# Optimization experiments

Hardware: AMD Instinct MI355X
Metric: run time of the kernel (lower is better)

Reference implementation:

```python
import jax, jax.numpy as jnp
import numpy as np

N = 3072      # number of EDU nodes in the document
H = 256       # opt.tree_hid_him
NREL = 18     # relation classes (hardcoded in rel_clf)
ALPHA = 0.25


def setup_inputs() -> dict:
    key = jax.random.key(0)
    ks = jax.random.split(key, 20)
    s = 0.02
    all_edus = jax.random.normal(ks[0], (1, N, H), jnp.float32)
    # dependency tree: child i (1..N-1) has parent < i
    children_ids = jnp.arange(1, N, dtype=jnp.int32)
    parents_ids = (jax.random.randint(ks[1], (N - 1,), 0, N) % jnp.maximum(children_ids, 1)).astype(jnp.int32)
    half = (N - 1) // 2
    left_adj = jnp.zeros((N, N), jnp.float32).at[parents_ids[:half], children_ids[:half]].set(1.0)
    right_adj = jnp.zeros((N, N), jnp.float32).at[parents_ids[half:], children_ids[half:]].set(1.0)
    rels = jax.random.randint(ks[2], (N - 1,), 1, NREL).astype(jnp.int32)  # all nonzero -> rels[rels!=0] == rels
    return dict(
        all_edus=all_edus,
        left_adj=left_adj,
        right_adj=right_adj,
        W_bilin=jax.random.normal(ks[3], (2, H, H), jnp.float32) * s,
        b_bilin=jnp.zeros((2,), jnp.float32),
        W_head=jax.random.normal(ks[4], (2, H), jnp.float32) * s,
        W_dep=jax.random.normal(ks[5], (2, H), jnp.float32) * s,
        Wr1=jax.random.normal(ks[6], (H, H), jnp.float32) * s,
        br1=jnp.zeros((H,), jnp.float32),
        Wr2=jax.random.normal(ks[7], (H, 1), jnp.float32) * s,
        br2=jnp.zeros((1,), jnp.float32),
        Wrel1=jax.random.normal(ks[8], (2 * H, H), jnp.float32) * s,
        brel1=jnp.zeros((H,), jnp.float32),
        Wrel2=jax.random.normal(ks[9], (H, NREL), jnp.float32) * s,
        brel2=jnp.zeros((NREL,), jnp.float32),
        children_ids=children_ids,
        parents_ids=parents_ids,
        rels=rels,
        true_root=0,
    )


def reference(all_edus, left_adj, right_adj, W_bilin, b_bilin, W_head, W_dep,
              Wr1, br1, Wr2, br2, Wrel1, brel1, Wrel2, brel2,
              children_ids, parents_ids, rels, true_root):
    x = all_edus[0]                                      # [N, H]
    # --- get_compat_matrix: compat[i, j, k] = bilin_k(h_i, h_j) + head_k(h_i) + dep_k(h_j) ---
    compat = (jnp.einsum('ih,khd,jd->ijk', x, W_bilin, x) + b_bilin
              + (x @ W_head.T)[:, None, :] + (x @ W_dep.T)[None, :, :])  # [N, N, 2]
    # --- root_clf ---
    g = jax.nn.gelu(x @ Wr1 + br1, approximate=False)
    root_scores = g @ Wr2 + br2                          # [N, 1]
    # --- logistic_loss (matrix-tree theorem) ---
    gold = (root_scores[true_root, 0]
            + jnp.sum(compat[:, :, 0] * left_adj)
            + jnp.sum(compat[:, :, 1] * right_adj))
    A = jnp.exp(compat).sum(axis=-1)                     # [N, N]
    lap = jnp.diag(A.sum(axis=0)) - A                    # diag of column sums (torch sum over dim=1)
    lap = lap.at[0, :].set(jnp.exp(root_scores[:, 0]))
    sign, logabs = jnp.linalg.slogdet(lap)
    logdet = jnp.where(sign > 0, logabs, jnp.nan)        # torch.logdet semantics
    notnan = ((~jnp.isnan(gold)) & (~jnp.isnan(logdet))).astype(lap.dtype)
    mask = (gold <= logdet * notnan).astype(lap.dtype)
    loss = (logdet - gold) * mask
    loss = jnp.where(jnp.isnan(loss), 0.0, loss)
    log_loss = ALPHA * loss
    # --- rels_loss: edge-indexed gather + MLP + CE(sum) ---
    feats = jnp.concatenate([x[parents_ids], x[children_ids]], axis=1)  # [E, 2H]
    h = jax.nn.gelu(feats @ Wrel1 + brel1, approximate=False)
    logits = h @ Wrel2 + brel2                           # [E, 18]
    logp = jax.nn.log_softmax(logits, axis=-1)
    ce = -jnp.sum(jnp.take_along_axis(logp, rels[:, None].astype(jnp.int32), axis=1))
    return log_loss + ce
```

## Files before the change

### kernel.cpp

```cpp
#include <hip/hip_runtime.h>
#include <math.h>

#define N 3072
#define H 256
#define NRELS 18
#define EDGES (N-1)
#define HALF ((N-1)/2)
#define NB 64
#define NSTEP (N/NB)

static const size_t OFF_M   = 0;
static const size_t OFF_Y   = (size_t)N*N;
static const size_t OFF_XH  = OFF_Y + (size_t)4*N*H;
static const size_t OFF_XD  = OFF_XH + (size_t)2*N;
static const size_t OFF_RS  = OFF_XD + (size_t)2*N;
static const size_t OFF_CS  = OFF_RS + (size_t)N;
static const size_t OFF_ACC = OFF_CS + (size_t)N;
static const size_t OFF_IAC = OFF_ACC + 8;

__device__ __forceinline__ float gelu_exact(float a){
    return 0.5f*a*(1.0f + erff(a*0.70710678118654752440f));
}

__global__ void k_init(float* cs, float* acc, int* iacc){
    int t = blockIdx.x*256 + threadIdx.x;
    if(t < N) cs[t] = 0.f;
    if(t < 8) acc[t] = 0.f;
    if(t < 4) iacc[t] = 0;
}

__global__ __launch_bounds__(256) void k_xhd(const float* __restrict__ x,
        const float* __restrict__ Wh, const float* __restrict__ Wd,
        float* __restrict__ xh, float* __restrict__ xd){
    __shared__ float xs[H];
    int i = blockIdx.x, t = threadIdx.x;
    xs[t] = x[(size_t)i*H + t];
    __syncthreads();
    int w = t >> 6, lane = t & 63;
    const float* Wrow = (w==0)? Wh : (w==1)? Wh+H : (w==2)? Wd : Wd+H;
    float s = 0.f;
    #pragma unroll
    for(int q=0;q<4;q++) s += xs[lane+64*q]*Wrow[lane+64*q];
    #pragma unroll
    for(int off=32;off>0;off>>=1) s += __shfl_down(s, off, 64);
    if(lane==0){ if(w<2) xh[i*2+w]=s; else xd[i*2+(w-2)]=s; }
}

__global__ __launch_bounds__(256) void k_root(const float* __restrict__ x,
        const float* __restrict__ Wr1, const float* __restrict__ br1,
        const float* __restrict__ Wr2, const float* __restrict__ br2,
        float* __restrict__ rs){
    __shared__ float xs[H];
    __shared__ float red[256];
    int i = blockIdx.x, t = threadIdx.x;
    xs[t] = x[(size_t)i*H + t];
    __syncthreads();
    float a = br1[t];
    for(int d=0; d<H; d++) a += xs[d]*Wr1[(size_t)d*H + t];
    red[t] = gelu_exact(a)*Wr2[t];
    __syncthreads();
    for(int s=128;s>0;s>>=1){ if(t<s) red[t]+=red[t+s]; __syncthreads(); }
    if(t==0) rs[i] = red[0] + br2[0];
}

__global__ __launch_bounds__(256) void k_mats(const float* __restrict__ x,
        const float* __restrict__ Wb, const float* __restrict__ Wrel1,
        float* __restrict__ Yout){
    __shared__ float xs[H];
    int i = blockIdx.x, m = blockIdx.y, t = threadIdx.x;
    xs[t] = x[(size_t)i*H + t];
    __syncthreads();
    const float* W = (m==0)? Wb : (m==1)? Wb + (size_t)H*H
                   : (m==2)? Wrel1 : Wrel1 + (size_t)H*H;
    float acc = 0.f;
    for(int h=0; h<H; h++) acc += xs[h]*W[(size_t)h*H + t];
    Yout[(size_t)m*N*H + (size_t)i*H + t] = acc;
}

__global__ __launch_bounds__(256) void k_compatA(
        const float* __restrict__ x, const float* __restrict__ Y0,
        const float* __restrict__ Y1, const float* __restrict__ xh,
        const float* __restrict__ xd, const float* __restrict__ bb,
        float* __restrict__ M){
    __shared__ float a0s[16][65], a1s[16][65], bs[16][65];
    int i0 = blockIdx.y*64, j0 = blockIdx.x*64;
    int t = threadIdx.x;
    int tx = t & 15, ty = t >> 4;
    float c0[4][4] = {}, c1[4][4] = {};
    for(int k0=0; k0<H; k0+=16){
        int kk = t & 15, r0 = t >> 4;
        for(int rr=r0; rr<64; rr+=16){
            a0s[kk][rr] = Y0[(size_t)(i0+rr)*H + k0+kk];
            a1s[kk][rr] = Y1[(size_t)(i0+rr)*H + k0+kk];
            bs [kk][rr] = x [(size_t)(j0+rr)*H + k0+kk];
        }
        __syncthreads();
        #pragma unroll
        for(int kk2=0; kk2<16; kk2++){
            float ar0[4], ar1[4], br[4];
            #pragma unroll
            for(int u=0;u<4;u++){ ar0[u]=a0s[kk2][ty*4+u]; ar1[u]=a1s[kk2][ty*4+u]; }
            #pragma unroll
            for(int v=0;v<4;v++) br[v]=bs[kk2][tx*4+v];
            #pragma unroll
            for(int u=0;u<4;u++)
                #pragma unroll
                for(int v=0;v<4;v++){ c0[u][v]+=ar0[u]*br[v]; c1[u][v]+=ar1[u]*br[v]; }
        }
        __syncthreads();
    }
    float b0 = bb[0], b1 = bb[1];
    #pragma unroll
    for(int u=0;u<4;u++){
        int i = i0 + ty*4 + u;
        float h0 = xh[2*i], h1 = xh[2*i+1];
        int pi = (i==0)? N-1 : i-1;
        #pragma unroll
        for(int v=0;v<4;v++){
            int j = j0 + tx*4 + v;
            int pj = (j==0)? N-1 : j-1;
            float cc0 = c0[u][v] + b0 + h0 + xd[2*j];
            float cc1 = c1[u][v] + b1 + h1 + xd[2*j+1];
            M[(size_t)pi*N + pj] = -(expf(cc0)+expf(cc1));
        }
    }
}

__global__ __launch_bounds__(256) void k_gold(const float* __restrict__ x,
        const float* __restrict__ Y, const float* __restrict__ xh,
        const float* __restrict__ xd, const float* __restrict__ bb,
        const int* __restrict__ par, const int* __restrict__ chi,
        float* __restrict__ acc){
    int w = threadIdx.x >> 6, lane = threadIdx.x & 63;
    int e = blockIdx.x*4 + w;
    if(e >= EDGES) return;
    int p = par[e], c = chi[e];
    int k = (e < HALF)? 0 : 1;
    const float* Yk = Y + (size_t)k*N*H;
    float s = 0.f;
    #pragma unroll
    for(int q=0;q<4;q++)
        s += Yk[(size_t)p*H + lane+64*q]*x[(size_t)c*H + lane+64*q];
    #pragma unroll
    for(int off=32;off>0;off>>=1) s += __shfl_down(s, off, 64);
    if(lane==0) atomicAdd(acc+0, s + bb[k] + xh[2*p+k] + xd[2*c+k]);
}

__global__ __launch_bounds__(256) void k_ce(
        const float* __restrict__ Pm, const float* __restrict__ Qm,
        const float* __restrict__ brel1, const float* __restrict__ Wrel2,
        const float* __restrict__ brel2, const int* __restrict__ par,
        const int* __restrict__ chi, const int* __restrict__ rels,
        float* __restrict__ acc){
    __shared__ float red[256][NRELS+1];
    int e = blockIdx.x, t = threadIdx.x;
    int p = par[e], c = chi[e];
    float a = Pm[(size_t)p*H + t] + Qm[(size_t)c*H + t] + brel1[t];
    float h = gelu_exact(a);
    #pragma unroll
    for(int r=0;r<NRELS;r++) red[t][r] = h*Wrel2[t*NRELS + r];
    __syncthreads();
    for(int s=128;s>0;s>>=1){
        if(t<s){
            #pragma unroll
            for(int r=0;r<NRELS;r++) red[t][r] += red[t+s][r];
        }
        __syncthreads();
    }
    if(t==0){
        int rsel = rels[e];
        float mx = -1e30f;
        for(int r=0;r<NRELS;r++) mx = fmaxf(mx, red[0][r]+brel2[r]);
        float se = 0.f;
        for(int r=0;r<NRELS;r++) se += expf(red[0][r]+brel2[r]-mx);
        float lse = mx + logf(se);
        atomicAdd(acc+2, lse - (red[0][rsel]+brel2[rsel]));
    }
}

__global__ __launch_bounds__(256) void k_colsum(const float* __restrict__ M,
        float* __restrict__ cs){
    int c = blockIdx.x*256 + threadIdx.x;
    int r0 = blockIdx.y*(N/16);
    float s = 0.f;
    for(int r=r0; r<r0+N/16; r++) s += M[(size_t)r*N + c];
    atomicAdd(cs+c, s);
}

__global__ __launch_bounds__(256) void k_fix(float* __restrict__ M,
        const float* __restrict__ cs, const float* __restrict__ rs){
    int c = blockIdx.x*256 + threadIdx.x;
    if(c < N-1) M[(size_t)c*N + c] -= cs[c];
    int oj = (c==N-1)? 0 : c+1;
    M[(size_t)(N-1)*N + c] = expf(rs[oj]);
}

__global__ __launch_bounds__(256) void k_lu_diag(float* __restrict__ M, int K0,
        float* __restrict__ acc, int* __restrict__ iacc){
    __shared__ float D[NB][NB+1];
    __shared__ float lcol[NB];
    int t = threadIdx.x;
    for(int e=t; e<NB*NB; e+=256){ int r=e>>6, c=e&63; D[r][c] = M[(size_t)(K0+r)*N + K0+c]; }
    __syncthreads();
    for(int j=0;j<NB;j++){
        if(t>j && t<NB){ float l = D[t][j]/D[j][j]; D[t][j]=l; lcol[t]=l; }
        __syncthreads();
        int ty = t>>4, tx = t&15;
        for(int ii=j+1+ty; ii<NB; ii+=16){
            float l = lcol[ii];
            for(int cc=j+1+tx; cc<NB; cc+=16) D[ii][cc] -= l*D[j][cc];
        }
        __syncthreads();
    }
    if(t==0){
        float s = 0.f; int neg=0, zer=0;
        for(int j=0;j<NB;j++){
            float v = D[j][j];
            s += logf(fabsf(v));
            if(v < 0.f) neg++;
            if(v == 0.f) zer++;
        }
        atomicAdd(acc+1, s);
        if(neg) atomicAdd(iacc+0, neg);
        if(zer) atomicAdd(iacc+1, zer);
    }
    __syncthreads();
    for(int e=t; e<NB*NB; e+=256){ int r=e>>6, c=e&63; M[(size_t)(K0+r)*N + K0+c] = D[r][c]; }
}

__global__ __launch_bounds__(128) void k_lu_panel(float* __restrict__ M, int K0){
    __shared__ float Dd[NB][NB+1];
    __shared__ float Tl[128][NB+1];
    int t = threadIdx.x;
    int m = N - K0 - NB;
    int nch = (m + 127)/128;
    for(int e=t; e<NB*NB; e+=128){ int r=e>>6, c=e&63; Dd[r][c] = M[(size_t)(K0+r)*N + K0+c]; }
    __syncthreads();
    if((int)blockIdx.x < nch){
        int base = K0 + NB + blockIdx.x*128;
        for(int e=t; e<128*NB; e+=128){ int rr=e>>6, cc=e&63;
            int row = base+rr; Tl[rr][cc] = (row<N)? M[(size_t)row*N + K0+cc] : 0.f; }
        __syncthreads();
        int row = base + t;
        if(row < N){
            float a[NB];
            #pragma unroll
            for(int c=0;c<NB;c++) a[c] = Tl[t][c];
            #pragma unroll
            for(int c=0;c<NB;c++){
                float xc = a[c]/Dd[c][c];
                a[c] = xc;
                #pragma unroll
                for(int cc=c+1;cc<NB;cc++) a[cc] -= xc*Dd[c][cc];
            }
            #pragma unroll
            for(int c=0;c<NB;c++) Tl[t][c] = a[c];
        }
        __syncthreads();
        for(int e=t; e<128*NB; e+=128){ int rr=e>>6, cc=e&63;
            int row2 = base+rr; if(row2<N) M[(size_t)row2*N + K0+cc] = Tl[rr][cc]; }
    } else {
        int cbase = K0 + NB + (blockIdx.x - nch)*128;
        for(int e=t; e<NB*128; e+=128){ int rr=e>>7, cc=e&127;
            int col = cbase+cc; Tl[cc][rr] = (col<N)? M[(size_t)(K0+rr)*N + col] : 0.f; }
        __syncthreads();
        int col = cbase + t;
        if(col < N){
            float a[NB];
            #pragma unroll
            for(int r=0;r<NB;r++) a[r] = Tl[t][r];
            #pragma unroll
            for(int r=0;r<NB;r++){
                float ur = a[r];
                #pragma unroll
                for(int rr=r+1;rr<NB;rr++) a[rr] -= ur*Dd[rr][r];
            }
            #pragma unroll
            for(int r=0;r<NB;r++) Tl[t][r] = a[r];
        }
        __syncthreads();
        for(int e=t; e<NB*128; e+=128){ int rr=e>>7, cc=e&127;
            int col2 = cbase+cc; if(col2<N) M[(size_t)(K0+rr)*N + col2] = Tl[cc][rr]; }
    }
}

__global__ __launch_bounds__(256) void k_lu_update(float* __restrict__ M, int K0){
    __shared__ float As[16][65], Bs[16][65];
    int base = K0 + NB;
    int ii0 = base + blockIdx.y*64;
    int jj0 = base + blockIdx.x*64;
    int t = threadIdx.x, tx = t&15, ty = t>>4;
    float c[4][4] = {};
    for(int k0=0; k0<NB; k0+=16){
        {
            int kk = t&15, r0 = t>>4;
            for(int rr=r0; rr<64; rr+=16)
                As[kk][rr] = M[(size_t)(ii0+rr)*N + K0+k0+kk];
        }
        {
            int cc = t&63, kr = t>>6;
            for(int k2=kr; k2<16; k2+=4)
                Bs[k2][cc] = M[(size_t)(K0+k0+k2)*N + jj0+cc];
        }
        __syncthreads();
        #pragma unroll
        for(int kk2=0; kk2<16; kk2++){
            float ar[4], br[4];
            #pragma unroll
            for(int u=0;u<4;u++) ar[u] = As[kk2][ty*4+u];
            #pragma unroll
            for(int v=0;v<4;v++) br[v] = Bs[kk2][tx*4+v];
            #pragma unroll
            for(int u=0;u<4;u++)
                #pragma unroll
                for(int v=0;v<4;v++) c[u][v] += ar[u]*br[v];
        }
        __syncthreads();
    }
    #pragma unroll
    for(int u=0;u<4;u++)
        #pragma unroll
        for(int v=0;v<4;v++){
            size_t idx = (size_t)(ii0+ty*4+u)*N + jj0+tx*4+v;
            M[idx] -= c[u][v];
        }
}

__global__ void k_final(const float* __restrict__ acc, const int* __restrict__ iacc,
        const float* __restrict__ rs, const int* __restrict__ troot,
        float* __restrict__ out){
    float gold = acc[0] + rs[troot[0]];
    float logabs = acc[1];
    bool pos = (iacc[1]==0) && ((iacc[0]&1)==0);
    float logdet = pos ? logabs : __builtin_nanf("");
    float notnan = (!isnan(gold) && !isnan(logdet)) ? 1.f : 0.f;
    float mv = logdet*notnan;
    float mask = (gold <= mv) ? 1.f : 0.f;
    float loss = (logdet - gold)*mask;
    if(isnan(loss)) loss = 0.f;
    out[0] = 0.25f*loss + acc[2];
}

extern "C" void kernel_launch(void* const* d_in, const int* in_sizes, int n_in,
                              void* d_out, int out_size, void* d_ws, size_t ws_size,
                              hipStream_t stream){
    const float* x     = (const float*)d_in[0];
    const float* Wb    = (const float*)d_in[3];
    const float* bb    = (const float*)d_in[4];
    const float* Wh    = (const float*)d_in[5];
    const float* Wd    = (const float*)d_in[6];
    const float* Wr1   = (const float*)d_in[7];
    const float* br1   = (const float*)d_in[8];
    const float* Wr2   = (const float*)d_in[9];
    const float* br2   = (const float*)d_in[10];
    const float* Wrel1 = (const float*)d_in[11];
    const float* brel1 = (const float*)d_in[12];
    const float* Wrel2 = (const float*)d_in[13];
    const float* brel2 = (const float*)d_in[14];
    const int* chi   = (const int*)d_in[15];
    const int* par   = (const int*)d_in[16];
    const int* rels  = (const int*)d_in[17];
    const int* troot = (const int*)d_in[18];

    float* ws = (float*)d_ws;
    float* M  = ws + OFF_M;
    float* Y  = ws + OFF_Y;
    float* Y0 = Y;
    float* Y1 = Y + (size_t)N*H;
    float* Pm = Y + (size_t)2*N*H;
    float* Qm = Y + (size_t)3*N*H;
    float* xh = ws + OFF_XH;
    float* xd = ws + OFF_XD;
    float* rs = ws + OFF_RS;
    float* cs = ws + OFF_CS;
    float* acc = ws + OFF_ACC;
    int*   iacc = (int*)(ws + OFF_IAC);
    float* out = (float*)d_out;

    k_init<<<N/256, 256, 0, stream>>>(cs, acc, iacc);
    k_xhd<<<N, 256, 0, stream>>>(x, Wh, Wd, xh, xd);
    k_root<<<N, 256, 0, stream>>>(x, Wr1, br1, Wr2, br2, rs);
    k_mats<<<dim3(N,4), 256, 0, stream>>>(x, Wb, Wrel1, Y);
    k_compatA<<<dim3(N/64, N/64), 256, 0, stream>>>(x, Y0, Y1, xh, xd, bb, M);
    k_gold<<<(EDGES+3)/4, 256, 0, stream>>>(x, Y, xh, xd, bb, par, chi, acc);
    k_ce<<<EDGES, 256, 0, stream>>>(Pm, Qm, brel1, Wrel2, brel2, par, chi, rels, acc);
    k_colsum<<<dim3(N/256, 16), 256, 0, stream>>>(M, cs);
    k_fix<<<N/256, 256, 0, stream>>>(M, cs, rs);

    k_lu_diag<<<1, 256, 0, stream>>>(M, 0, acc, iacc);
    for(int kb=0; kb<NSTEP-1; kb++){
        int K0 = kb*NB;
        int m  = N - K0 - NB;
        int nch = (m + 127)/128;
        k_lu_panel<<<2*nch, 128, 0, stream>>>(M, K0);
        dim3 g(m/64, m/64);
        k_lu_update<<<g, 256, 0, stream>>>(M, K0);
        k_lu_diag<<<1, 256, 0, stream>>>(M, K0+NB, acc, iacc);
    }
    k_final<<<1, 1, 0, stream>>>(acc, iacc, rs, troot, out);
}
```

Baseline: 5.498 ms.

## Replace LU panel triangular solves with explicit block inverses and fuse diag factorization

The 64x64 diagonal block factorization now also builds explicit inverses of U and L and stores them in the no-longer-needed Y scratch area. The panel step becomes a small GEMM against those inverses instead of per-thread sequential triangular solves. The next diagonal block is factored inside block (0,0) of the trailing-update kernel, which removes one launch per step. Loads are vectorized with float4. In exchange, explicit inversion is slightly less numerically stable, and block (0,0) now lengthens the update kernel's critical path.

```diff
diff --git a/kernel.cpp b/kernel.cpp
--- a/kernel.cpp
+++ b/kernel.cpp
@@ -195,27 +195,26 @@
     M[(size_t)(N-1)*N + c] = expf(rs[oj]);
 }
 
-__global__ __launch_bounds__(256) void k_lu_diag(float* __restrict__ M, int K0,
-        float* __restrict__ acc, int* __restrict__ iacc){
-    __shared__ float D[NB][NB+1];
-    __shared__ float lcol[NB];
+__device__ __forceinline__ void factor_invert_64(
+        float (*Ds)[NB+1], float (*Xs)[NB+1], float (*Ys)[NB+1],
+        float* __restrict__ Uinv, float* __restrict__ Linv,
+        float* __restrict__ acc, int* __restrict__ iacc,
+        float* lcol ){
     int t = threadIdx.x;
-    for(int e=t; e<NB*NB; e+=256){ int r=e>>6, c=e&63; D[r][c] = M[(size_t)(K0+r)*N + K0+c]; }
-    __syncthreads();
     for(int j=0;j<NB;j++){
-        if(t>j && t<NB){ float l = D[t][j]/D[j][j]; D[t][j]=l; lcol[t]=l; }
+        if(t>j && t<NB){ float l = Ds[t][j]/Ds[j][j]; Ds[t][j]=l; lcol[t]=l; }
         __syncthreads();
         int ty = t>>4, tx = t&15;
         for(int ii=j+1+ty; ii<NB; ii+=16){
             float l = lcol[ii];
-            for(int cc=j+1+tx; cc<NB; cc+=16) D[ii][cc] -= l*D[j][cc];
+            for(int cc=j+1+tx; cc<NB; cc+=16) Ds[ii][cc] -= l*Ds[j][cc];
         }
         __syncthreads();
     }
     if(t==0){
         float s = 0.f; int neg=0, zer=0;
         for(int j=0;j<NB;j++){
-            float v = D[j][j];
+            float v = Ds[j][j];
             s += logf(fabsf(v));
             if(v < 0.f) neg++;
             if(v == 0.f) zer++;
@@ -225,105 +224,161 @@
         if(zer) atomicAdd(iacc+1, zer);
     }
     __syncthreads();
-    for(int e=t; e<NB*NB; e+=256){ int r=e>>6, c=e&63; M[(size_t)(K0+r)*N + K0+c] = D[r][c]; }
-}
-
-__global__ __launch_bounds__(128) void k_lu_panel(float* __restrict__ M, int K0){
-    __shared__ float Dd[NB][NB+1];
-    __shared__ float Tl[128][NB+1];
+    if(t < NB){
+        int c = t;
+        for(int r=NB-1;r>=0;r--){
+            float v;
+            if(r > c) v = 0.f;
+            else {
+                v = (r==c)? 1.f : 0.f;
+                for(int j=r+1;j<=c;j++) v -= Ds[r][j]*Xs[j][c];
+                v /= Ds[r][r];
+            }
+            Xs[r][c] = v;
+        }
+        for(int r=0;r<NB;r++) Uinv[r*NB+c] = Xs[r][c];
+    } else if(t < 2*NB){
+        int c = t - NB;
+        for(int r=0;r<NB;r++){
+            float v;
+            if(r < c) v = 0.f;
+            else if(r == c) v = 1.f;
+            else {
+                v = 0.f;
+                for(int j=c;j<r;j++) v -= Ds[r][j]*Ys[j][c];
+            }
+            Ys[r][c] = v;
+        }
+        for(int r=0;r<NB;r++) Linv[r*NB+c] = Ys[r][c];
+    }
+}
+
+__global__ __launch_bounds__(256) void k_lu_diag0(const float* __restrict__ M,
+        float* __restrict__ Uinv, float* __restrict__ Linv,
+        float* __restrict__ acc, int* __restrict__ iacc){
+    __shared__ float Ds[NB][NB+1], Xs[NB][NB+1], Ys[NB][NB+1];
+    __shared__ float lcol[NB];
     int t = threadIdx.x;
-    int m = N - K0 - NB;
-    int nch = (m + 127)/128;
-    for(int e=t; e<NB*NB; e+=128){ int r=e>>6, c=e&63; Dd[r][c] = M[(size_t)(K0+r)*N + K0+c]; }
-    __syncthreads();
-    if((int)blockIdx.x < nch){
-        int base = K0 + NB + blockIdx.x*128;
-        for(int e=t; e<128*NB; e+=128){ int rr=e>>6, cc=e&63;
-            int row = base+rr; Tl[rr][cc] = (row<N)? M[(size_t)row*N + K0+cc] : 0.f; }
-        __syncthreads();
-        int row = base + t;
-        if(row < N){
-            float a[NB];
-            #pragma unroll
-            for(int c=0;c<NB;c++) a[c] = Tl[t][c];
-            #pragma unroll
-            for(int c=0;c<NB;c++){
-                float xc = a[c]/Dd[c][c];
-                a[c] = xc;
-                #pragma unroll
-                for(int cc=c+1;cc<NB;cc++) a[cc] -= xc*Dd[c][cc];
-            }
-            #pragma unroll
-            for(int c=0;c<NB;c++) Tl[t][c] = a[c];
-        }
-        __syncthreads();
-        for(int e=t; e<128*NB; e+=128){ int rr=e>>6, cc=e&63;
-            int row2 = base+rr; if(row2<N) M[(size_t)row2*N + K0+cc] = Tl[rr][cc]; }
+    for(int e=t; e<NB*NB; e+=256){ int r=e>>6, c=e&63; Ds[r][c] = M[(size_t)r*N + c]; }
+    __syncthreads();
+    factor_invert_64(Ds, Xs, Ys, Uinv, Linv, acc, iacc, lcol);
+}
+
+__global__ __launch_bounds__(256) void k_lu_panel(float* __restrict__ M, int K0,
+        const float* __restrict__ Uinv, const float* __restrict__ Linv){
+    __shared__ float As[NB][NB+1], Bs[NB][NB+1];
+    int t = threadIdx.x;
+    int base = K0 + NB;
+    int nt = (N - base)/NB;
+    bool isL = ((int)blockIdx.x < nt);
+    int bi = isL ? blockIdx.x : blockIdx.x - nt;
+
+    int lr = t >> 4, lc4 = (t & 15)*4;
+    if(isL){
+        int ii0 = base + bi*NB;
+        #pragma unroll
+        for(int q=0;q<4;q++){
+            int r = lr + 16*q;
+            float4 v = *(const float4*)&M[(size_t)(ii0+r)*N + K0 + lc4];
+            As[r][lc4]=v.x; As[r][lc4+1]=v.y; As[r][lc4+2]=v.z; As[r][lc4+3]=v.w;
+            float4 u = *(const float4*)&Uinv[r*NB + lc4];
+            Bs[r][lc4]=u.x; Bs[r][lc4+1]=u.y; Bs[r][lc4+2]=u.z; Bs[r][lc4+3]=u.w;
+        }
     } else {
-        int cbase = K0 + NB + (blockIdx.x - nch)*128;
-        for(int e=t; e<NB*128; e+=128){ int rr=e>>7, cc=e&127;
-            int col = cbase+cc; Tl[cc][rr] = (col<N)? M[(size_t)(K0+rr)*N + col] : 0.f; }
-        __syncthreads();
-        int col = cbase + t;
-        if(col < N){
-            float a[NB];
-            #pragma unroll
-            for(int r=0;r<NB;r++) a[r] = Tl[t][r];
-            #pragma unroll
-            for(int r=0;r<NB;r++){
-                float ur = a[r];
-                #pragma unroll
-                for(int rr=r+1;rr<NB;rr++) a[rr] -= ur*Dd[rr][r];
-            }
-            #pragma unroll
-            for(int r=0;r<NB;r++) Tl[t][r] = a[r];
-        }
-        __syncthreads();
-        for(int e=t; e<NB*128; e+=128){ int rr=e>>7, cc=e&127;
-            int col2 = cbase+cc; if(col2<N) M[(size_t)(K0+rr)*N + col2] = Tl[cc][rr]; }
-    }
-}
-
-__global__ __launch_bounds__(256) void k_lu_update(float* __restrict__ M, int K0){
-    __shared__ float As[16][65], Bs[16][65];
+        int jj0 = base + bi*NB;
+        #pragma unroll
+        for(int q=0;q<4;q++){
+            int r = lr + 16*q;
+            float4 v = *(const float4*)&M[(size_t)(K0+r)*N + jj0 + lc4];
+            Bs[r][lc4]=v.x; Bs[r][lc4+1]=v.y; Bs[r][lc4+2]=v.z; Bs[r][lc4+3]=v.w;
+            float4 u = *(const float4*)&Linv[r*NB + lc4];
+            As[r][lc4]=u.x; As[r][lc4+1]=u.y; As[r][lc4+2]=u.z; As[r][lc4+3]=u.w;
+        }
+    }
+    __syncthreads();
+    int tx = t & 15, ty = t >> 4;
+    float c[4][4] = {};
+    #pragma unroll 8
+    for(int k=0;k<NB;k++){
+        float ar[4], br[4];
+        #pragma unroll
+        for(int u=0;u<4;u++) ar[u] = As[ty*4+u][k];
+        #pragma unroll
+        for(int v=0;v<4;v++) br[v] = Bs[k][tx*4+v];
+        #pragma unroll
+        for(int u=0;u<4;u++)
+            #pragma unroll
+            for(int v=0;v<4;v++) c[u][v] += ar[u]*br[v];
+    }
+    #pragma unroll
+    for(int u=0;u<4;u++){
+        float4 w = make_float4(c[u][0], c[u][1], c[u][2], c[u][3]);
+        size_t idx;
+        if(isL){
+            int ii0 = base + bi*NB;
+            idx = (size_t)(ii0 + ty*4+u)*N + K0 + tx*4;
+        } else {
+            int jj0 = base + bi*NB;
+            idx = (size_t)(K0 + ty*4+u)*N + jj0 + tx*4;
+        }
+        *(float4*)&M[idx] = w;
+    }
+}
+
+__global__ __launch_bounds__(256) void k_lu_update(float* __restrict__ M, int K0,
+        float* __restrict__ Uinv, float* __restrict__ Linv,
+        float* __restrict__ acc, int* __restrict__ iacc){
+    __shared__ float As[NB][NB+1], Bs[NB][NB+1], Ys[NB][NB+1];
+    __shared__ float lcol[NB];
+    int t = threadIdx.x;
     int base = K0 + NB;
-    int ii0 = base + blockIdx.y*64;
-    int jj0 = base + blockIdx.x*64;
-    int t = threadIdx.x, tx = t&15, ty = t>>4;
+    int ii0 = base + blockIdx.y*NB;
+    int jj0 = base + blockIdx.x*NB;
+
+    int lr = t >> 4, lc4 = (t & 15)*4;
+    #pragma unroll
+    for(int q=0;q<4;q++){
+        int r = lr + 16*q;
+        float4 a = *(const float4*)&M[(size_t)(ii0+r)*N + K0 + lc4];
+        As[r][lc4]=a.x; As[r][lc4+1]=a.y; As[r][lc4+2]=a.z; As[r][lc4+3]=a.w;
+        float4 b = *(const float4*)&M[(size_t)(K0+r)*N + jj0 + lc4];
+        Bs[r][lc4]=b.x; Bs[r][lc4+1]=b.y; Bs[r][lc4+2]=b.z; Bs[r][lc4+3]=b.w;
+    }
+    __syncthreads();
+    int tx = t & 15, ty = t >> 4;
     float c[4][4] = {};
-    for(int k0=0; k0<NB; k0+=16){
-        {
-            int kk = t&15, r0 = t>>4;
-            for(int rr=r0; rr<64; rr+=16)
-                As[kk][rr] = M[(size_t)(ii0+rr)*N + K0+k0+kk];
-        }
-        {
-            int cc = t&63, kr = t>>6;
-            for(int k2=kr; k2<16; k2+=4)
-                Bs[k2][cc] = M[(size_t)(K0+k0+k2)*N + jj0+cc];
-        }
-        __syncthreads();
-        #pragma unroll
-        for(int kk2=0; kk2<16; kk2++){
-            float ar[4], br[4];
-            #pragma unroll
-            for(int u=0;u<4;u++) ar[u] = As[kk2][ty*4+u];
-            #pragma unroll
-            for(int v=0;v<4;v++) br[v] = Bs[kk2][tx*4+v];
-            #pragma unroll
-            for(int u=0;u<4;u++)
-                #pragma unroll
-                for(int v=0;v<4;v++) c[u][v] += ar[u]*br[v];
-        }
-        __syncthreads();
-    }
-    #pragma unroll
-    for(int u=0;u<4;u++)
-        #pragma unroll
-        for(int v=0;v<4;v++){
-            size_t idx = (size_t)(ii0+ty*4+u)*N + jj0+tx*4+v;
-            M[idx] -= c[u][v];
-        }
+    #pragma unroll 8
+    for(int k=0;k<NB;k++){
+        float ar[4], br[4];
+        #pragma unroll
+        for(int u=0;u<4;u++) ar[u] = As[ty*4+u][k];
+        #pragma unroll
+        for(int v=0;v<4;v++) br[v] = Bs[k][tx*4+v];
+        #pragma unroll
+        for(int u=0;u<4;u++)
+            #pragma unroll
+            for(int v=0;v<4;v++) c[u][v] += ar[u]*br[v];
+    }
+    float res[4][4];
+    #pragma unroll
+    for(int u=0;u<4;u++){
+        size_t idx = (size_t)(ii0 + ty*4+u)*N + jj0 + tx*4;
+        float4 oc = *(const float4*)&M[idx];
+        res[u][0]=oc.x - c[u][0]; res[u][1]=oc.y - c[u][1];
+        res[u][2]=oc.z - c[u][2]; res[u][3]=oc.w - c[u][3];
+        *(float4*)&M[idx] = make_float4(res[u][0], res[u][1], res[u][2], res[u][3]);
+    }
+    if(blockIdx.x==0 && blockIdx.y==0){
+        __syncthreads();
+        float (*Ds)[NB+1] = As;
+        float (*Xs)[NB+1] = Bs;
+        #pragma unroll
+        for(int u=0;u<4;u++)
+            #pragma unroll
+            for(int v=0;v<4;v++) Ds[ty*4+u][tx*4+v] = res[u][v];
+        __syncthreads();
+        factor_invert_64(Ds, Xs, Ys, Uinv, Linv, acc, iacc, lcol);
+    }
 }
 
 __global__ void k_final(const float* __restrict__ acc, const int* __restrict__ iacc,
@@ -375,6 +430,8 @@
     float* cs = ws + OFF_CS;
     float* acc = ws + OFF_ACC;
     int*   iacc = (int*)(ws + OFF_IAC);
+    float* Uinv = Y;
+    float* Linv = Y + NB*NB;
     float* out = (float*)d_out;
 
     k_init<<<N/256, 256, 0, stream>>>(cs, acc, iacc);
@@ -387,15 +444,14 @@
     k_colsum<<<dim3(N/256, 16), 256, 0, stream>>>(M, cs);
     k_fix<<<N/256, 256, 0, stream>>>(M, cs, rs);
 
-    k_lu_diag<<<1, 256, 0, stream>>>(M, 0, acc, iacc);
+    k_lu_diag0<<<1, 256, 0, stream>>>(M, Uinv, Linv, acc, iacc);
     for(int kb=0; kb<NSTEP-1; kb++){
         int K0 = kb*NB;
         int m  = N - K0 - NB;
-        int nch = (m + 127)/128;
-        k_lu_panel<<<2*nch, 128, 0, stream>>>(M, K0);
-        dim3 g(m/64, m/64);
-        k_lu_update<<<g, 256, 0, stream>>>(M, K0);
-        k_lu_diag<<<1, 256, 0, stream>>>(M, K0+NB, acc, iacc);
+        int nt = m/NB;
+        k_lu_panel<<<2*nt, 256, 0, stream>>>(M, K0, Uinv, Linv);
+        dim3 g(nt, nt);
+        k_lu_update<<<g, 256, 0, stream>>>(M, K0, Uinv, Linv, acc, iacc);
     }
     k_final<<<1, 1, 0, stream>>>(acc, iacc, rs, troot, out);
 }
```

New measurement: 7.187 ms. 1.31x slower.
